# Performance work log

Hardware: AMD Instinct MI355X
Metric: run time of the kernel (lower is better)

The kernel has to match this reference:

```python
import jax, jax.numpy as jnp
import numpy as np

NUM_SLOTS = 8
SLOT_DIM = 256
ITERS = 3
EPS = 1e-8
SCALE = SLOT_DIM ** -0.5


def _ln(x, g, b, eps=1e-5):
    m = jnp.mean(x, axis=-1, keepdims=True)
    v = jnp.mean(jnp.square(x - m), axis=-1, keepdims=True)
    return (x - m) * jax.lax.rsqrt(v + eps) * g + b


def setup_inputs() -> dict:
    key = jax.random.key(0)
    ks = jax.random.split(key, 16)
    b, n, c = 32, 1024, 256
    d = SLOT_DIM
    def xavier(k, shape):
        fan_in, fan_out = shape[1], shape[0]
        lim = np.sqrt(6.0 / (fan_in + fan_out))
        return jax.random.uniform(k, shape, jnp.float32, -lim, lim)
    lim_mu = np.sqrt(6.0 / (1 + d))
    return {
        "inputs": jax.random.normal(ks[0], (b, n, c), jnp.float32),
        "noise": jax.random.normal(ks[1], (b, NUM_SLOTS, d), jnp.float32),
        "slots_mu": jax.random.uniform(ks[2], (1, 1, d), jnp.float32, -lim_mu, lim_mu),
        "slots_log_sigma": jax.random.uniform(ks[3], (1, 1, d), jnp.float32, -lim_mu, lim_mu),
        "Wq": xavier(ks[4], (d, d)),
        "Wk": xavier(ks[5], (d, c)),
        "Wv": xavier(ks[6], (d, c)),
        "gru_wih": xavier(ks[7], (3 * d, d)),
        "gru_whh": xavier(ks[8], (3 * d, d)),
        "gru_bih": jnp.zeros((3 * d,), jnp.float32),
        "gru_bhh": jnp.zeros((3 * d,), jnp.float32),
        "mlp_w1": xavier(ks[9], (4 * d, d)),
        "mlp_b1": jnp.zeros((4 * d,), jnp.float32),
        "mlp_w2": xavier(ks[10], (d, 4 * d)),
        "mlp_b2": jnp.zeros((d,), jnp.float32),
        "ln_in_g": jnp.ones((c,), jnp.float32),
        "ln_in_b": jnp.zeros((c,), jnp.float32),
        "ln_s_g": jnp.ones((d,), jnp.float32),
        "ln_s_b": jnp.zeros((d,), jnp.float32),
        "ln_ff_g": jnp.ones((d,), jnp.float32),
        "ln_ff_b": jnp.zeros((d,), jnp.float32),
    }


def reference(inputs, noise, slots_mu, slots_log_sigma, Wq, Wk, Wv,
              gru_wih, gru_whh, gru_bih, gru_bhh,
              mlp_w1, mlp_b1, mlp_w2, mlp_b2,
              ln_in_g, ln_in_b, ln_s_g, ln_s_b, ln_ff_g, ln_ff_b):
    b = inputs.shape[0]
    d = SLOT_DIM
    # slots ~ N(mu, sigma) reparameterized with given noise
    slots = slots_mu + jnp.exp(slots_log_sigma) * noise  # [b, S, d]
    x = _ln(inputs, ln_in_g, ln_in_b)
    k = jnp.einsum('bnc,dc->bnd', x, Wk)
    v = jnp.einsum('bnc,dc->bnd', x, Wv)
    for _ in range(ITERS):
        slots_prev = slots
        s = _ln(slots, ln_s_g, ln_s_b)
        q = jnp.einsum('bid,ed->bie', s, Wq)
        dots = jnp.einsum('bid,bjd->bij', q, k) * SCALE  # [b, S, n]
        attn = jax.nn.softmax(dots, axis=1) + EPS         # softmax over slots
        attn = attn / jnp.sum(attn, axis=-1, keepdims=True)
        updates = jnp.einsum('bjd,bij->bid', v, attn)      # [b, S, d]
        # GRUCell: x=updates, h=slots_prev (flattened over batch*slots)
        u = updates.reshape(-1, d)
        h = slots_prev.reshape(-1, d)
        gi = u @ gru_wih.T + gru_bih
        gh = h @ gru_whh.T + gru_bhh
        i_r, i_z, i_n = jnp.split(gi, 3, axis=-1)
        h_r, h_z, h_n = jnp.split(gh, 3, axis=-1)
        r = jax.nn.sigmoid(i_r + h_r)
        z = jax.nn.sigmoid(i_z + h_z)
        nn_ = jnp.tanh(i_n + r * h_n)
        slots = ((1.0 - z) * nn_ + z * h).reshape(b, -1, d)
        ff = _ln(slots, ln_ff_g, ln_ff_b)
        ff = jax.nn.relu(ff @ mlp_w1.T + mlp_b1) @ mlp_w2.T + mlp_b2
        slots = slots + ff
    return slots
```

## Files before the change

### kernel.cpp

```cpp
#include <hip/hip_runtime.h>


typedef __attribute__((ext_vector_type(8))) __bf16 bf16x8;
typedef __attribute__((ext_vector_type(4))) float  f32x4;

#define MFMA16(a, b, c) __builtin_amdgcn_mfma_f32_16x16x32_bf16((a), (b), (c), 0, 0, 0)

static __device__ __forceinline__ unsigned short f2bf(float f) {
    unsigned int x = __float_as_uint(f);
    x = (x + 0x7fffu + ((x >> 16) & 1u)) >> 16;
    return (unsigned short)x;
}
static __device__ __forceinline__ float bf2f(unsigned short u) {
    return __uint_as_float((unsigned int)u << 16);
}
static __device__ __forceinline__ float bflo(unsigned int x) {
    return __uint_as_float(x << 16);
}
static __device__ __forceinline__ float bfhi(unsigned int x) {
    return __uint_as_float(x & 0xffff0000u);
}

struct Params {
    const float *inputs, *noise, *mu, *ls;
    const float *Wq, *Wk, *Wv, *wih, *whh, *bih, *bhh, *w1, *b1, *w2, *b2;
    const float *ln_in_g, *ln_in_b, *ln_s_g, *ln_s_b, *ln_ff_g, *ln_ff_b;
    float* out;
    unsigned short *x_bf, *kvW_bf, *Wq_bf, *wih_bf, *whh_bf, *w1_bf, *w2_bf;
    unsigned short *kv_bf, *u_bf, *h_bf, *ff_bf, *h1_bf;
    float *slots, *q, *upart, *rspart, *gi, *gh, *opart;
};

static __device__ void qgemm(const Params& p, const unsigned short (&u)[16][264], int r0) {
    const int t = threadIdx.x, w = t >> 6, lane = t & 63;
    const int lr = lane & 15, lq = lane >> 4;
    f32x4 acc[4] = {};
    for (int k0 = 0; k0 < 256; k0 += 32) {
        bf16x8 a = *(const bf16x8*)&u[lr][k0 + lq * 8];
        #pragma unroll
        for (int j = 0; j < 4; ++j) {
            bf16x8 bv = *(const bf16x8*)(p.Wq_bf + (size_t)(w * 64 + j * 16 + lr) * 256 + k0 + lq * 8);
            acc[j] = MFMA16(a, bv, acc[j]);
        }
    }
    #pragma unroll
    for (int j = 0; j < 4; ++j)
        #pragma unroll
        for (int r = 0; r < 4; ++r)
            p.q[(size_t)(r0 + lq * 4 + r) * 256 + w * 64 + j * 16 + lr] = acc[j][r];
}

__global__ __launch_bounds__(256) void k_prep(Params p) {
    const int bid = blockIdx.x, t = threadIdx.x;
    for (int gid = bid * 256 + t; gid < 1179648; gid += 4608 * 256) {
        if      (gid <   65536) p.kvW_bf[gid]          = f2bf(p.Wk[gid]);
        else if (gid <  131072) p.kvW_bf[gid]          = f2bf(p.Wv[gid -   65536]);
        else if (gid <  196608) p.Wq_bf[gid - 131072]  = f2bf(p.Wq[gid -  131072]);
        else if (gid <  393216) p.wih_bf[gid - 196608] = f2bf(p.wih[gid - 196608]);
        else if (gid <  589824) p.whh_bf[gid - 393216] = f2bf(p.whh[gid - 393216]);
        else if (gid <  851968) p.w1_bf[gid - 589824]  = f2bf(p.w1[gid -  589824]);
        else if (gid < 1114112) p.w2_bf[gid - 851968]  = f2bf(p.w2[gid -  851968]);
        else {
            const int i = gid - 1114112;
            const int d = i & 255;
            p.slots[i] = p.mu[d] + expf(p.ls[d]) * p.noise[i];
        }
    }
    const int wid  = (bid * 256 + t) >> 6;
    const int lane = t & 63;
    const float g0 = p.ln_in_g[lane * 4 + 0], g1 = p.ln_in_g[lane * 4 + 1];
    const float g2 = p.ln_in_g[lane * 4 + 2], g3 = p.ln_in_g[lane * 4 + 3];
    const float b0 = p.ln_in_b[lane * 4 + 0], b1 = p.ln_in_b[lane * 4 + 1];
    const float b2 = p.ln_in_b[lane * 4 + 2], b3 = p.ln_in_b[lane * 4 + 3];
    #pragma unroll 2
    for (int row = wid; row < 32768; row += 18432) {
        float4 v = *(const float4*)(p.inputs + (size_t)row * 256 + lane * 4);
        float s  = v.x + v.y + v.z + v.w;
        float ss = v.x * v.x + v.y * v.y + v.z * v.z + v.w * v.w;
        #pragma unroll
        for (int o = 1; o < 64; o <<= 1) { s += __shfl_xor(s, o); ss += __shfl_xor(ss, o); }
        float mean = s * (1.f / 256.f);
        float var  = ss * (1.f / 256.f) - mean * mean;
        float rstd = rsqrtf(var + 1e-5f);
        ushort4 o4;
        o4.x = f2bf((v.x - mean) * rstd * g0 + b0);
        o4.y = f2bf((v.y - mean) * rstd * g1 + b1);
        o4.z = f2bf((v.z - mean) * rstd * g2 + b2);
        o4.w = f2bf((v.w - mean) * rstd * g3 + b3);
        *(ushort4*)(p.x_bf + (size_t)row * 256 + lane * 4) = o4;
    }
}

union KvSmem {
    struct { unsigned short As[128 * 32], Bs[128 * 32]; } g;
    unsigned short u[16][264];
};

__global__ __launch_bounds__(256) void k_kv(Params p) {
    __shared__ KvSmem sm;
    const int bid = blockIdx.x, t = threadIdx.x;
    if (bid < 1024) {
        const int m0 = (bid >> 2) * 128, n0 = (bid & 3) * 128;
        const int wave = t >> 6, lane = t & 63;
        const int qr = (wave >> 1) * 64, qc = (wave & 1) * 64;
        const int lr = lane & 15, lq = lane >> 4;
        f32x4 acc[4][4] = {};
        const int sr = t >> 2, sl = t & 3, gk = sl * 8;
        const int wsl0 = (sl ^ ((sr >> 1) & 3)) * 8;
        const int wsl1 = (sl ^ (((sr + 64) >> 1) & 3)) * 8;
        for (int k0 = 0; k0 < 256; k0 += 32) {
            __syncthreads();
            uint4 a0 = *(const uint4*)(p.x_bf   + (size_t)(m0 + sr)      * 256 + k0 + gk);
            uint4 a1 = *(const uint4*)(p.x_bf   + (size_t)(m0 + sr + 64) * 256 + k0 + gk);
            uint4 b0 = *(const uint4*)(p.kvW_bf + (size_t)(n0 + sr)      * 256 + k0 + gk);
            uint4 b1 = *(const uint4*)(p.kvW_bf + (size_t)(n0 + sr + 64) * 256 + k0 + gk);
            *(uint4*)(sm.g.As + sr * 32 + wsl0) = a0;
            *(uint4*)(sm.g.As + (sr + 64) * 32 + wsl1) = a1;
            *(uint4*)(sm.g.Bs + sr * 32 + wsl0) = b0;
            *(uint4*)(sm.g.Bs + (sr + 64) * 32 + wsl1) = b1;
            __syncthreads();
            bf16x8 af[4], bv[4];
            #pragma unroll
            for (int i = 0; i < 4; i++) {
                const int ra = qr + i * 16 + lr;
                af[i] = *(const bf16x8*)(sm.g.As + ra * 32 + ((lq ^ ((ra >> 1) & 3)) * 8));
            }
            #pragma unroll
            for (int i = 0; i < 4; i++) {
                const int rb = qc + i * 16 + lr;
                bv[i] = *(const bf16x8*)(sm.g.Bs + rb * 32 + ((lq ^ ((rb >> 1) & 3)) * 8));
            }
            #pragma unroll
            for (int i = 0; i < 4; i++)
                #pragma unroll
                for (int j = 0; j < 4; j++)
                    acc[i][j] = MFMA16(af[i], bv[j], acc[i][j]);
        }
        #pragma unroll
        for (int i = 0; i < 4; i++)
            #pragma unroll
            for (int j = 0; j < 4; j++) {
                const int col = n0 + qc + j * 16 + lr;
                #pragma unroll
                for (int r = 0; r < 4; r++) {
                    const int rw = m0 + qr + i * 16 + lq * 4 + r;
                    p.kv_bf[(size_t)rw * 512 + col] = f2bf(acc[i][j][r]);
                }
            }
    } else {
        const int r0 = (bid - 1024) * 16;
        const int row16 = t >> 4, sub = t & 15;
        float vals[16]; float s = 0.f, ss = 0.f;
        #pragma unroll
        for (int k = 0; k < 16; k += 4) {
            float4 v = *(const float4*)(p.slots + (size_t)(r0 + row16) * 256 + sub * 16 + k);
            vals[k] = v.x; vals[k + 1] = v.y; vals[k + 2] = v.z; vals[k + 3] = v.w;
            s += v.x + v.y + v.z + v.w;
            ss += v.x * v.x + v.y * v.y + v.z * v.z + v.w * v.w;
        }
        #pragma unroll
        for (int m = 1; m < 16; m <<= 1) { s += __shfl_xor(s, m); ss += __shfl_xor(ss, m); }
        const float mean = s * (1.f / 256.f);
        const float var  = ss * (1.f / 256.f) - mean * mean;
        const float rstd = rsqrtf(var + 1e-5f);
        #pragma unroll
        for (int k = 0; k < 16; ++k) {
            const int c = sub * 16 + k;
            sm.u[row16][c] = f2bf((vals[k] - mean) * rstd * p.ln_s_g[c] + p.ln_s_b[c]);
        }
        __syncthreads();
        qgemm(p, sm.u, r0);
    }
}

__global__ __launch_bounds__(256) void k_attn(Params p) {
    __shared__ float q_s[8][260];
    __shared__ float sc[8][68];
    const int bid = blockIdx.x, t = threadIdx.x;
    const int b = bid >> 4, chunk = bid & 15, j0 = chunk * 64;
    {
        const int i = t >> 5, c0 = (t & 31) * 8;
        const float* qr = p.q + (size_t)(b * 8 + i) * 256 + c0;
        *(float4*)&q_s[i][c0]     = *(const float4*)(qr);
        *(float4*)&q_s[i][c0 + 4] = *(const float4*)(qr + 4);
    }
    __syncthreads();
    {
        const int i = t & 7, jj = t >> 3;
        const float4* qrow = (const float4*)&q_s[i][0];
        #pragma unroll 1
        for (int g = 0; g < 2; ++g) {
            const int jl = g * 32 + jj;
            const uint4* krow = (const uint4*)(p.kv_bf + ((size_t)b * 1024 + j0 + jl) * 512);
            float a0 = 0, a1 = 0, a2 = 0, a3 = 0;
            #pragma unroll 8
            for (int dd = 0; dd < 32; ++dd) {
                uint4 kk = krow[dd];
                float4 q0 = qrow[2 * dd], q1 = qrow[2 * dd + 1];
                a0 += q0.x * bflo(kk.x); a1 += q0.y * bfhi(kk.x);
                a2 += q0.z * bflo(kk.y); a3 += q0.w * bfhi(kk.y);
                a0 += q1.x * bflo(kk.z); a1 += q1.y * bfhi(kk.z);
                a2 += q1.z * bflo(kk.w); a3 += q1.w * bfhi(kk.w);
            }
            sc[i][jl] = (a0 + a1 + a2 + a3) * 0.0625f;
        }
    }
    __syncthreads();
    if (t < 64) {
        float v[8], m = -1e30f;
        #pragma unroll
        for (int ii = 0; ii < 8; ++ii) { v[ii] = sc[ii][t]; m = fmaxf(m, v[ii]); }
        float s = 0.f;
        #pragma unroll
        for (int ii = 0; ii < 8; ++ii) { v[ii] = __expf(v[ii] - m); s += v[ii]; }
        const float inv = 1.f / s;
        #pragma unroll
        for (int ii = 0; ii < 8; ++ii) sc[ii][t] = v[ii] * inv + 1e-8f;
    }
    __syncthreads();
    if (t < 8) {
        float s = 0.f;
        for (int jl = 0; jl < 64; ++jl) s += sc[t][jl];
        p.rspart[((size_t)b * 16 + chunk) * 8 + t] = s;
    }
    {
        float acc[8] = {};
        const unsigned short* vbase = p.kv_bf + ((size_t)b * 1024 + j0) * 512 + 256 + t;
        #pragma unroll 8
        for (int jl = 0; jl < 64; ++jl) {
            const float vv = bf2f(vbase[(size_t)jl * 512]);
            #pragma unroll
            for (int ii = 0; ii < 8; ++ii) acc[ii] += sc[ii][jl] * vv;
        }
        float* up = p.upart + (((size_t)b * 16 + chunk) * 8) * 256 + t;
        #pragma unroll
        for (int ii = 0; ii < 8; ++ii) up[ii * 256] = acc[ii];
    }
}

__global__ __launch_bounds__(256) void k_u2b(Params p) {
    const int row = blockIdx.x, t = threadIdx.x;
    const int b = row >> 3, i = row & 7;
    float acc = 0.f, rs = 0.f;
    #pragma unroll
    for (int c = 0; c < 16; ++c) {
        acc += p.upart[(((size_t)b * 16 + c) * 8 + i) * 256 + t];
        rs  += p.rspart[((size_t)b * 16 + c) * 8 + i];
    }
    const float inv = 1.f / rs;
    p.u_bf[(size_t)row * 256 + t] = f2bf(acc * inv);
    p.h_bf[(size_t)row * 256 + t] = f2bf(p.slots[(size_t)row * 256 + t]);
}

__global__ __launch_bounds__(256) void k_gates(Params p) {
    __shared__ unsigned short As[64 * 32], Bs[64 * 32];
    const int m0 = blockIdx.x * 64;
    const int n0g = blockIdx.y * 64;
    const bool isGi = n0g < 768;
    const int n0 = isGi ? n0g : n0g - 768;
    const unsigned short* A = isGi ? p.u_bf : p.h_bf;
    const unsigned short* B = isGi ? p.wih_bf : p.whh_bf;
    float* C = isGi ? p.gi : p.gh;
    const int t = threadIdx.x, wave = t >> 6, lane = t & 63;
    const int lr = lane & 15, lq = lane >> 4;
    f32x4 acc[4] = {};
    const int sr = t >> 2, sl = t & 3, gk = sl * 8;
    const int wsl = (sl ^ ((sr >> 1) & 3)) * 8;
    for (int k0 = 0; k0 < 256; k0 += 32) {
        __syncthreads();
        uint4 a0 = *(const uint4*)(A + (size_t)(m0 + sr) * 256 + k0 + gk);
        uint4 b0 = *(const uint4*)(B + (size_t)(n0 + sr) * 256 + k0 + gk);
        *(uint4*)(As + sr * 32 + wsl) = a0;
        *(uint4*)(Bs + sr * 32 + wsl) = b0;
        __syncthreads();
        const int ra = wave * 16 + lr;
        bf16x8 af = *(const bf16x8*)(As + ra * 32 + ((lq ^ ((ra >> 1) & 3)) * 8));
        #pragma unroll
        for (int j = 0; j < 4; ++j) {
            const int rb = j * 16 + lr;
            bf16x8 bv = *(const bf16x8*)(Bs + rb * 32 + ((lq ^ ((rb >> 1) & 3)) * 8));
            acc[j] = MFMA16(af, bv, acc[j]);
        }
    }
    #pragma unroll
    for (int j = 0; j < 4; ++j) {
        const int col = n0 + j * 16 + lr;
        #pragma unroll
        for (int r = 0; r < 4; ++r) {
            const int row = m0 + wave * 16 + lq * 4 + r;
            C[(size_t)row * 768 + col] = acc[j][r];
        }
    }
}

__global__ __launch_bounds__(256) void k_gruln(Params p) {
    __shared__ float red[8];
    const int row = blockIdx.x, t = threadIdx.x;
    const float* gir = p.gi + (size_t)row * 768;
    const float* ghr = p.gh + (size_t)row * 768;
    const float ir  = gir[t]       + p.bih[t];
    const float iz  = gir[256 + t] + p.bih[256 + t];
    const float in_ = gir[512 + t] + p.bih[512 + t];
    const float hr  = ghr[t]       + p.bhh[t];
    const float hz  = ghr[256 + t] + p.bhh[256 + t];
    const float hn  = ghr[512 + t] + p.bhh[512 + t];
    const float r = 1.f / (1.f + __expf(-(ir + hr)));
    const float z = 1.f / (1.f + __expf(-(iz + hz)));
    const float n = tanhf(in_ + r * hn);
    const float h = p.slots[(size_t)row * 256 + t];
    const float s = (1.f - z) * n + z * h;
    p.slots[(size_t)row * 256 + t] = s;
    float sm = s, ssq = s * s;
    #pragma unroll
    for (int o = 32; o > 0; o >>= 1) { sm += __shfl_down(sm, o); ssq += __shfl_down(ssq, o); }
    if ((t & 63) == 0) { red[t >> 6] = sm; red[4 + (t >> 6)] = ssq; }
    __syncthreads();
    const float S  = red[0] + red[1] + red[2] + red[3];
    const float SS = red[4] + red[5] + red[6] + red[7];
    const float mean = S * (1.f / 256.f);
    const float var  = SS * (1.f / 256.f) - mean * mean;
    const float rstd = rsqrtf(var + 1e-5f);
    p.ff_bf[(size_t)row * 256 + t] = f2bf((s - mean) * rstd * p.ln_ff_g[t] + p.ln_ff_b[t]);
}

__global__ __launch_bounds__(256) void k_mlp1(Params p) {
    __shared__ unsigned short As[64 * 32], Bs[64 * 32];
    const int m0 = blockIdx.x * 64, n0 = blockIdx.y * 64;
    const int t = threadIdx.x, wave = t >> 6, lane = t & 63;
    const int lr = lane & 15, lq = lane >> 4;
    f32x4 acc[4] = {};
    const int sr = t >> 2, sl = t & 3, gk = sl * 8;
    const int wsl = (sl ^ ((sr >> 1) & 3)) * 8;
    for (int k0 = 0; k0 < 256; k0 += 32) {
        __syncthreads();
        uint4 a0 = *(const uint4*)(p.ff_bf + (size_t)(m0 + sr) * 256 + k0 + gk);
        uint4 b0 = *(const uint4*)(p.w1_bf + (size_t)(n0 + sr) * 256 + k0 + gk);
        *(uint4*)(As + sr * 32 + wsl) = a0;
        *(uint4*)(Bs + sr * 32 + wsl) = b0;
        __syncthreads();
        const int ra = wave * 16 + lr;
        bf16x8 af = *(const bf16x8*)(As + ra * 32 + ((lq ^ ((ra >> 1) & 3)) * 8));
        #pragma unroll
        for (int j = 0; j < 4; ++j) {
            const int rb = j * 16 + lr;
            bf16x8 bv = *(const bf16x8*)(Bs + rb * 32 + ((lq ^ ((rb >> 1) & 3)) * 8));
            acc[j] = MFMA16(af, bv, acc[j]);
        }
    }
    #pragma unroll
    for (int j = 0; j < 4; ++j) {
        const int col = n0 + j * 16 + lr;
        const float bb = p.b1[col];
        #pragma unroll
        for (int r = 0; r < 4; ++r) {
            const int row = m0 + wave * 16 + lq * 4 + r;
            p.h1_bf[(size_t)row * 1024 + col] = f2bf(fmaxf(acc[j][r] + bb, 0.f));
        }
    }
}

__global__ __launch_bounds__(256) void k_out(Params p) {
    __shared__ unsigned short a_s[16][264];
    const int t = threadIdx.x;
    const int r0 = blockIdx.x * 16, kb = blockIdx.y * 256;
    const int row16 = t >> 4, sub = t & 15;
    {
        const unsigned short* src = p.h1_bf + (size_t)(r0 + row16) * 1024 + kb + sub * 16;
        *(uint4*)&a_s[row16][sub * 16]     = *(const uint4*)(src);
        *(uint4*)&a_s[row16][sub * 16 + 8] = *(const uint4*)(src + 8);
    }
    __syncthreads();
    const int w = t >> 6, lane = t & 63;
    const int lr = lane & 15, lq = lane >> 4;
    f32x4 acc[4] = {};
    for (int k0 = 0; k0 < 256; k0 += 32) {
        bf16x8 a = *(const bf16x8*)&a_s[lr][k0 + lq * 8];
        #pragma unroll
        for (int j = 0; j < 4; ++j) {
            bf16x8 bv = *(const bf16x8*)(p.w2_bf + (size_t)(w * 64 + j * 16 + lr) * 1024 + kb + k0 + lq * 8);
            acc[j] = MFMA16(a, bv, acc[j]);
        }
    }
    #pragma unroll
    for (int j = 0; j < 4; ++j)
        #pragma unroll
        for (int r = 0; r < 4; ++r)
            p.opart[((size_t)blockIdx.y * 256 + r0 + lq * 4 + r) * 256 + w * 64 + j * 16 + lr] = acc[j][r];
}

template<int LAST>
__global__ __launch_bounds__(256) void k_lnq(Params p) {
    __shared__ unsigned short u[16][264];
    const int t = threadIdx.x;
    const int r0 = blockIdx.x * 16;
    const int row16 = t >> 4, sub = t & 15;
    float vals[16]; float s_ = 0.f, ss = 0.f;
    #pragma unroll
    for (int k = 0; k < 16; ++k) {
        const int c = sub * 16 + k;
        const size_t ridx = (size_t)(r0 + row16) * 256 + c;
        float v = p.opart[(size_t)(r0 + row16) * 256 + c]
                + p.opart[((size_t)256 + r0 + row16) * 256 + c]
                + p.opart[((size_t)512 + r0 + row16) * 256 + c]
                + p.opart[((size_t)768 + r0 + row16) * 256 + c]
                + p.b2[c] + p.slots[ridx];
        p.slots[ridx] = v;
        if (LAST) p.out[ridx] = v;
        vals[k] = v; s_ += v; ss += v * v;
    }
    if (LAST) return;
    #pragma unroll
    for (int m = 1; m < 16; m <<= 1) { s_ += __shfl_xor(s_, m); ss += __shfl_xor(ss, m); }
    const float mean = s_ * (1.f / 256.f);
    const float var  = ss * (1.f / 256.f) - mean * mean;
    const float rstd = rsqrtf(var + 1e-5f);
    #pragma unroll
    for (int k = 0; k < 16; ++k) {
        const int c = sub * 16 + k;
        u[row16][c] = f2bf((vals[k] - mean) * rstd * p.ln_s_g[c] + p.ln_s_b[c]);
    }
    __syncthreads();
    qgemm(p, u, r0);
}

extern "C" void kernel_launch(void* const* d_in, const int* in_sizes, int n_in,
                              void* d_out, int out_size, void* d_ws, size_t ws_size,
                              hipStream_t stream)
{
    (void)in_sizes; (void)n_in; (void)out_size; (void)ws_size;

    Params prm;
    prm.inputs  = (const float*)d_in[0];
    prm.noise   = (const float*)d_in[1];
    prm.mu      = (const float*)d_in[2];
    prm.ls      = (const float*)d_in[3];
    prm.Wq      = (const float*)d_in[4];
    prm.Wk      = (const float*)d_in[5];
    prm.Wv      = (const float*)d_in[6];
    prm.wih     = (const float*)d_in[7];
    prm.whh     = (const float*)d_in[8];
    prm.bih     = (const float*)d_in[9];
    prm.bhh     = (const float*)d_in[10];
    prm.w1      = (const float*)d_in[11];
    prm.b1      = (const float*)d_in[12];
    prm.w2      = (const float*)d_in[13];
    prm.b2      = (const float*)d_in[14];
    prm.ln_in_g = (const float*)d_in[15];
    prm.ln_in_b = (const float*)d_in[16];
    prm.ln_s_g  = (const float*)d_in[17];
    prm.ln_s_b  = (const float*)d_in[18];
    prm.ln_ff_g = (const float*)d_in[19];
    prm.ln_ff_b = (const float*)d_in[20];
    prm.out     = (float*)d_out;

    char* ptr = (char*)d_ws;
    auto alloc = [&](size_t bytes) -> char* {
        char* r = ptr; ptr += (bytes + 255) & ~(size_t)255; return r;
    };
    prm.x_bf   = (unsigned short*)alloc((size_t)32768 * 256 * 2);
    prm.kv_bf  = (unsigned short*)alloc((size_t)32768 * 512 * 2);
    prm.kvW_bf = (unsigned short*)alloc(512 * 256 * 2);
    prm.Wq_bf  = (unsigned short*)alloc(256 * 256 * 2);
    prm.wih_bf = (unsigned short*)alloc(768 * 256 * 2);
    prm.whh_bf = (unsigned short*)alloc(768 * 256 * 2);
    prm.w1_bf  = (unsigned short*)alloc(1024 * 256 * 2);
    prm.w2_bf  = (unsigned short*)alloc(256 * 1024 * 2);
    prm.slots  = (float*)         alloc(256 * 256 * 4);
    prm.q      = (float*)         alloc(256 * 256 * 4);
    prm.upart  = (float*)         alloc((size_t)32 * 16 * 8 * 256 * 4);
    prm.rspart = (float*)         alloc(32 * 16 * 8 * 4);
    prm.u_bf   = (unsigned short*)alloc(256 * 256 * 2);
    prm.h_bf   = (unsigned short*)alloc(256 * 256 * 2);
    prm.gi     = (float*)         alloc(256 * 768 * 4);
    prm.gh     = (float*)         alloc(256 * 768 * 4);
    prm.ff_bf  = (unsigned short*)alloc(256 * 256 * 2);
    prm.h1_bf  = (unsigned short*)alloc(256 * 1024 * 2);
    prm.opart  = (float*)         alloc((size_t)4 * 256 * 256 * 4);

    k_prep<<<4608, 256, 0, stream>>>(prm);
    k_kv  <<<1040, 256, 0, stream>>>(prm);
    for (int it = 0; it < 3; ++it) {
        k_attn <<<512, 256, 0, stream>>>(prm);
        k_u2b  <<<256, 256, 0, stream>>>(prm);
        k_gates<<<dim3(4, 24), 256, 0, stream>>>(prm);
        k_gruln<<<256, 256, 0, stream>>>(prm);
        k_mlp1 <<<dim3(4, 16), 256, 0, stream>>>(prm);
        k_out  <<<dim3(16, 4), 256, 0, stream>>>(prm);
        if (it < 2) k_lnq<0><<<16, 256, 0, stream>>>(prm);
        else        k_lnq<1><<<16, 256, 0, stream>>>(prm);
    }
}
```

Baseline: 293.1 us.

## Fuse slot-iteration kernels using last-block atomic reductions

```diff
diff --git a/kernel.cpp b/kernel.cpp
--- a/kernel.cpp
+++ b/kernel.cpp
@@ -27,8 +27,9 @@
     const float *ln_in_g, *ln_in_b, *ln_s_g, *ln_s_b, *ln_ff_g, *ln_ff_b;
     float* out;
     unsigned short *x_bf, *kvW_bf, *Wq_bf, *wih_bf, *whh_bf, *w1_bf, *w2_bf;
-    unsigned short *kv_bf, *u_bf, *h_bf, *ff_bf, *h1_bf;
-    float *slots, *q, *upart, *rspart, *gi, *gh, *opart;
+    unsigned short *kv_bf, *u_bf, *h_bf, *h1_bf;
+    float *slots, *smid, *q, *upart, *rspart, *gi, *gh, *opart;
+    unsigned* cnt;
 };
 
 static __device__ void qgemm(const Params& p, const unsigned short (&u)[16][264], int r0) {
@@ -166,6 +167,7 @@
         #pragma unroll
         for (int k = 0; k < 16; ++k) {
             const int c = sub * 16 + k;
+            p.h_bf[(size_t)(r0 + row16) * 256 + c] = f2bf(vals[k]);
             sm.u[row16][c] = f2bf((vals[k] - mean) * rstd * p.ln_s_g[c] + p.ln_s_b[c]);
         }
         __syncthreads();
@@ -173,11 +175,12 @@
     }
 }
 
-__global__ __launch_bounds__(256) void k_attn(Params p) {
+__global__ __launch_bounds__(256) void k_attn(Params p, int it) {
     __shared__ float q_s[8][260];
-    __shared__ float sc[8][68];
+    __shared__ float sc[8][132];
+    __shared__ int lastFlag;
     const int bid = blockIdx.x, t = threadIdx.x;
-    const int b = bid >> 4, chunk = bid & 15, j0 = chunk * 64;
+    const int b = bid >> 3, chunk = bid & 7, j0 = chunk * 128;
     {
         const int i = t >> 5, c0 = (t & 31) * 8;
         const float* qr = p.q + (size_t)(b * 8 + i) * 256 + c0;
@@ -189,7 +192,7 @@
         const int i = t & 7, jj = t >> 3;
         const float4* qrow = (const float4*)&q_s[i][0];
         #pragma unroll 1
-        for (int g = 0; g < 2; ++g) {
+        for (int g = 0; g < 4; ++g) {
             const int jl = g * 32 + jj;
             const uint4* krow = (const uint4*)(p.kv_bf + ((size_t)b * 1024 + j0 + jl) * 512);
             float a0 = 0, a1 = 0, a2 = 0, a3 = 0;
@@ -206,7 +209,7 @@
         }
     }
     __syncthreads();
-    if (t < 64) {
+    if (t < 128) {
         float v[8], m = -1e30f;
         #pragma unroll
         for (int ii = 0; ii < 8; ++ii) { v[ii] = sc[ii][t]; m = fmaxf(m, v[ii]); }
@@ -220,36 +223,43 @@
     __syncthreads();
     if (t < 8) {
         float s = 0.f;
-        for (int jl = 0; jl < 64; ++jl) s += sc[t][jl];
-        p.rspart[((size_t)b * 16 + chunk) * 8 + t] = s;
+        for (int jl = 0; jl < 128; ++jl) s += sc[t][jl];
+        p.rspart[((size_t)b * 8 + chunk) * 8 + t] = s;
     }
     {
         float acc[8] = {};
         const unsigned short* vbase = p.kv_bf + ((size_t)b * 1024 + j0) * 512 + 256 + t;
         #pragma unroll 8
-        for (int jl = 0; jl < 64; ++jl) {
+        for (int jl = 0; jl < 128; ++jl) {
             const float vv = bf2f(vbase[(size_t)jl * 512]);
             #pragma unroll
             for (int ii = 0; ii < 8; ++ii) acc[ii] += sc[ii][jl] * vv;
         }
-        float* up = p.upart + (((size_t)b * 16 + chunk) * 8) * 256 + t;
+        float* up = p.upart + (((size_t)b * 8 + chunk) * 8) * 256 + t;
         #pragma unroll
         for (int ii = 0; ii < 8; ++ii) up[ii * 256] = acc[ii];
     }
-}
-
-__global__ __launch_bounds__(256) void k_u2b(Params p) {
-    const int row = blockIdx.x, t = threadIdx.x;
-    const int b = row >> 3, i = row & 7;
-    float acc = 0.f, rs = 0.f;
-    #pragma unroll
-    for (int c = 0; c < 16; ++c) {
-        acc += p.upart[(((size_t)b * 16 + c) * 8 + i) * 256 + t];
-        rs  += p.rspart[((size_t)b * 16 + c) * 8 + i];
-    }
-    const float inv = 1.f / rs;
-    p.u_bf[(size_t)row * 256 + t] = f2bf(acc * inv);
-    p.h_bf[(size_t)row * 256 + t] = f2bf(p.slots[(size_t)row * 256 + t]);
+    __syncthreads();
+    if (t == 0) {
+        unsigned my = __hip_atomic_fetch_add(p.cnt + b * 16, 1u,
+                                             __ATOMIC_ACQ_REL, __HIP_MEMORY_SCOPE_AGENT);
+        const int isl = (my == (unsigned)(8 * (it + 1) - 1));
+        if (isl) __builtin_amdgcn_fence(__ATOMIC_ACQUIRE, "agent");
+        lastFlag = isl;
+    }
+    __syncthreads();
+    if (!lastFlag) return;
+    #pragma unroll
+    for (int i = 0; i < 8; ++i) {
+        float acc = 0.f, rs = 0.f;
+        #pragma unroll
+        for (int c = 0; c < 8; ++c) {
+            acc += p.upart[(((size_t)b * 8 + c) * 8 + i) * 256 + t];
+            rs  += p.rspart[((size_t)b * 8 + c) * 8 + i];
+        }
+        const float inv = 1.f / rs;
+        p.u_bf[(size_t)(b * 8 + i) * 256 + t] = f2bf(acc * inv);
+    }
 }
 
 __global__ __launch_bounds__(256) void k_gates(Params p) {
@@ -293,74 +303,68 @@
     }
 }
 
-__global__ __launch_bounds__(256) void k_gruln(Params p) {
-    __shared__ float red[8];
-    const int row = blockIdx.x, t = threadIdx.x;
-    const float* gir = p.gi + (size_t)row * 768;
-    const float* ghr = p.gh + (size_t)row * 768;
-    const float ir  = gir[t]       + p.bih[t];
-    const float iz  = gir[256 + t] + p.bih[256 + t];
-    const float in_ = gir[512 + t] + p.bih[512 + t];
-    const float hr  = ghr[t]       + p.bhh[t];
-    const float hz  = ghr[256 + t] + p.bhh[256 + t];
-    const float hn  = ghr[512 + t] + p.bhh[512 + t];
-    const float r = 1.f / (1.f + __expf(-(ir + hr)));
-    const float z = 1.f / (1.f + __expf(-(iz + hz)));
-    const float n = tanhf(in_ + r * hn);
-    const float h = p.slots[(size_t)row * 256 + t];
-    const float s = (1.f - z) * n + z * h;
-    p.slots[(size_t)row * 256 + t] = s;
-    float sm = s, ssq = s * s;
-    #pragma unroll
-    for (int o = 32; o > 0; o >>= 1) { sm += __shfl_down(sm, o); ssq += __shfl_down(ssq, o); }
-    if ((t & 63) == 0) { red[t >> 6] = sm; red[4 + (t >> 6)] = ssq; }
-    __syncthreads();
-    const float S  = red[0] + red[1] + red[2] + red[3];
-    const float SS = red[4] + red[5] + red[6] + red[7];
-    const float mean = S * (1.f / 256.f);
-    const float var  = SS * (1.f / 256.f) - mean * mean;
+__global__ __launch_bounds__(256) void k_mlp1f(Params p) {
+    __shared__ unsigned short ff[16][264];
+    const int t = threadIdx.x;
+    const int r0 = blockIdx.x * 16, nb = blockIdx.y * 256;
+    const int row16 = t >> 4, sub = t & 15;
+    const int grow = r0 + row16;
+    const float* gir = p.gi + (size_t)grow * 768;
+    const float* ghr = p.gh + (size_t)grow * 768;
+    float vals[16]; float s_ = 0.f, ss = 0.f;
+    #pragma unroll
+    for (int k = 0; k < 16; ++k) {
+        const int c = sub * 16 + k;
+        const float ir  = gir[c]       + p.bih[c];
+        const float iz  = gir[256 + c] + p.bih[256 + c];
+        const float in_ = gir[512 + c] + p.bih[512 + c];
+        const float hr  = ghr[c]       + p.bhh[c];
+        const float hz  = ghr[256 + c] + p.bhh[256 + c];
+        const float hn  = ghr[512 + c] + p.bhh[512 + c];
+        const float r = 1.f / (1.f + __expf(-(ir + hr)));
+        const float z = 1.f / (1.f + __expf(-(iz + hz)));
+        const float n = tanhf(in_ + r * hn);
+        const float h = p.slots[(size_t)grow * 256 + c];
+        const float s = (1.f - z) * n + z * h;
+        if (blockIdx.y == 0) p.smid[(size_t)grow * 256 + c] = s;
+        vals[k] = s; s_ += s; ss += s * s;
+    }
+    #pragma unroll
+    for (int m = 1; m < 16; m <<= 1) { s_ += __shfl_xor(s_, m); ss += __shfl_xor(ss, m); }
+    const float mean = s_ * (1.f / 256.f);
+    const float var  = ss * (1.f / 256.f) - mean * mean;
     const float rstd = rsqrtf(var + 1e-5f);
-    p.ff_bf[(size_t)row * 256 + t] = f2bf((s - mean) * rstd * p.ln_ff_g[t] + p.ln_ff_b[t]);
-}
-
-__global__ __launch_bounds__(256) void k_mlp1(Params p) {
-    __shared__ unsigned short As[64 * 32], Bs[64 * 32];
-    const int m0 = blockIdx.x * 64, n0 = blockIdx.y * 64;
-    const int t = threadIdx.x, wave = t >> 6, lane = t & 63;
-    const int lr = lane & 15, lq = lane >> 4;
+    #pragma unroll
+    for (int k = 0; k < 16; ++k) {
+        const int c = sub * 16 + k;
+        ff[row16][c] = f2bf((vals[k] - mean) * rstd * p.ln_ff_g[c] + p.ln_ff_b[c]);
+    }
+    __syncthreads();
+    const int w = t >> 6, lane = t & 63, lr = lane & 15, lq = lane >> 4;
     f32x4 acc[4] = {};
-    const int sr = t >> 2, sl = t & 3, gk = sl * 8;
-    const int wsl = (sl ^ ((sr >> 1) & 3)) * 8;
     for (int k0 = 0; k0 < 256; k0 += 32) {
-        __syncthreads();
-        uint4 a0 = *(const uint4*)(p.ff_bf + (size_t)(m0 + sr) * 256 + k0 + gk);
-        uint4 b0 = *(const uint4*)(p.w1_bf + (size_t)(n0 + sr) * 256 + k0 + gk);
-        *(uint4*)(As + sr * 32 + wsl) = a0;
-        *(uint4*)(Bs + sr * 32 + wsl) = b0;
-        __syncthreads();
-        const int ra = wave * 16 + lr;
-        bf16x8 af = *(const bf16x8*)(As + ra * 32 + ((lq ^ ((ra >> 1) & 3)) * 8));
+        bf16x8 a = *(const bf16x8*)&ff[lr][k0 + lq * 8];
         #pragma unroll
         for (int j = 0; j < 4; ++j) {
-            const int rb = j * 16 + lr;
-            bf16x8 bv = *(const bf16x8*)(Bs + rb * 32 + ((lq ^ ((rb >> 1) & 3)) * 8));
-            acc[j] = MFMA16(af, bv, acc[j]);
+            bf16x8 bv = *(const bf16x8*)(p.w1_bf + (size_t)(nb + w * 64 + j * 16 + lr) * 256 + k0 + lq * 8);
+            acc[j] = MFMA16(a, bv, acc[j]);
         }
     }
     #pragma unroll
     for (int j = 0; j < 4; ++j) {
-        const int col = n0 + j * 16 + lr;
+        const int col = nb + w * 64 + j * 16 + lr;
         const float bb = p.b1[col];
         #pragma unroll
-        for (int r = 0; r < 4; ++r) {
-            const int row = m0 + wave * 16 + lq * 4 + r;
-            p.h1_bf[(size_t)row * 1024 + col] = f2bf(fmaxf(acc[j][r] + bb, 0.f));
-        }
-    }
-}
-
-__global__ __launch_bounds__(256) void k_out(Params p) {
+        for (int r = 0; r < 4; ++r)
+            p.h1_bf[(size_t)(r0 + lq * 4 + r) * 1024 + col] = f2bf(fmaxf(acc[j][r] + bb, 0.f));
+    }
+}
+
+template<int LAST>
+__global__ __launch_bounds__(256) void k_out(Params p, int it) {
     __shared__ unsigned short a_s[16][264];
+    __shared__ unsigned short u[16][264];
+    __shared__ int lastFlag;
     const int t = threadIdx.x;
     const int r0 = blockIdx.x * 16, kb = blockIdx.y * 256;
     const int row16 = t >> 4, sub = t & 15;
@@ -370,8 +374,7 @@
         *(uint4*)&a_s[row16][sub * 16 + 8] = *(const uint4*)(src + 8);
     }
     __syncthreads();
-    const int w = t >> 6, lane = t & 63;
-    const int lr = lane & 15, lq = lane >> 4;
+    const int w = t >> 6, lane = t & 63, lr = lane & 15, lq = lane >> 4;
     f32x4 acc[4] = {};
     for (int k0 = 0; k0 < 256; k0 += 32) {
         bf16x8 a = *(const bf16x8*)&a_s[lr][k0 + lq * 8];
@@ -386,26 +389,31 @@
         #pragma unroll
         for (int r = 0; r < 4; ++r)
             p.opart[((size_t)blockIdx.y * 256 + r0 + lq * 4 + r) * 256 + w * 64 + j * 16 + lr] = acc[j][r];
-}
-
-template<int LAST>
-__global__ __launch_bounds__(256) void k_lnq(Params p) {
-    __shared__ unsigned short u[16][264];
-    const int t = threadIdx.x;
-    const int r0 = blockIdx.x * 16;
-    const int row16 = t >> 4, sub = t & 15;
+    __syncthreads();
+    if (t == 0) {
+        unsigned my = __hip_atomic_fetch_add(p.cnt + (32 + blockIdx.x) * 16, 1u,
+                                             __ATOMIC_ACQ_REL, __HIP_MEMORY_SCOPE_AGENT);
+        const int isl = (my == (unsigned)(4 * (it + 1) - 1));
+        if (isl) __builtin_amdgcn_fence(__ATOMIC_ACQUIRE, "agent");
+        lastFlag = isl;
+    }
+    __syncthreads();
+    if (!lastFlag) return;
     float vals[16]; float s_ = 0.f, ss = 0.f;
     #pragma unroll
     for (int k = 0; k < 16; ++k) {
         const int c = sub * 16 + k;
         const size_t ridx = (size_t)(r0 + row16) * 256 + c;
-        float v = p.opart[(size_t)(r0 + row16) * 256 + c]
+        float v = p.opart[ridx]
                 + p.opart[((size_t)256 + r0 + row16) * 256 + c]
                 + p.opart[((size_t)512 + r0 + row16) * 256 + c]
                 + p.opart[((size_t)768 + r0 + row16) * 256 + c]
-                + p.b2[c] + p.slots[ridx];
-        p.slots[ridx] = v;
-        if (LAST) p.out[ridx] = v;
+                + p.b2[c] + p.smid[ridx];
+        if (LAST) { p.out[ridx] = v; }
+        else {
+            p.slots[ridx] = v;
+            p.h_bf[ridx]  = f2bf(v);
+        }
         vals[k] = v; s_ += v; ss += v * v;
     }
     if (LAST) return;
@@ -457,6 +465,7 @@
     auto alloc = [&](size_t bytes) -> char* {
         char* r = ptr; ptr += (bytes + 255) & ~(size_t)255; return r;
     };
+    prm.cnt    = (unsigned*)      alloc(4096);
     prm.x_bf   = (unsigned short*)alloc((size_t)32768 * 256 * 2);
     prm.kv_bf  = (unsigned short*)alloc((size_t)32768 * 512 * 2);
     prm.kvW_bf = (unsigned short*)alloc(512 * 256 * 2);
@@ -466,27 +475,25 @@
     prm.w1_bf  = (unsigned short*)alloc(1024 * 256 * 2);
     prm.w2_bf  = (unsigned short*)alloc(256 * 1024 * 2);
     prm.slots  = (float*)         alloc(256 * 256 * 4);
+    prm.smid   = (float*)         alloc(256 * 256 * 4);
     prm.q      = (float*)         alloc(256 * 256 * 4);
-    prm.upart  = (float*)         alloc((size_t)32 * 16 * 8 * 256 * 4);
-    prm.rspart = (float*)         alloc(32 * 16 * 8 * 4);
+    prm.upart  = (float*)         alloc((size_t)32 * 8 * 8 * 256 * 4);
+    prm.rspart = (float*)         alloc(32 * 8 * 8 * 4);
     prm.u_bf   = (unsigned short*)alloc(256 * 256 * 2);
     prm.h_bf   = (unsigned short*)alloc(256 * 256 * 2);
     prm.gi     = (float*)         alloc(256 * 768 * 4);
     prm.gh     = (float*)         alloc(256 * 768 * 4);
-    prm.ff_bf  = (unsigned short*)alloc(256 * 256 * 2);
     prm.h1_bf  = (unsigned short*)alloc(256 * 1024 * 2);
     prm.opart  = (float*)         alloc((size_t)4 * 256 * 256 * 4);
 
+    hipMemsetAsync(prm.cnt, 0, 4096, stream);
     k_prep<<<4608, 256, 0, stream>>>(prm);
     k_kv  <<<1040, 256, 0, stream>>>(prm);
     for (int it = 0; it < 3; ++it) {
-        k_attn <<<512, 256, 0, stream>>>(prm);
-        k_u2b  <<<256, 256, 0, stream>>>(prm);
+        k_attn <<<256, 256, 0, stream>>>(prm, it);
         k_gates<<<dim3(4, 24), 256, 0, stream>>>(prm);
-        k_gruln<<<256, 256, 0, stream>>>(prm);
-        k_mlp1 <<<dim3(4, 16), 256, 0, stream>>>(prm);
-        k_out  <<<dim3(16, 4), 256, 0, stream>>>(prm);
-        if (it < 2) k_lnq<0><<<16, 256, 0, stream>>>(prm);
-        else        k_lnq<1><<<16, 256, 0, stream>>>(prm);
-    }
-}
+        k_mlp1f<<<dim3(16, 4), 256, 0, stream>>>(prm);
+        if (it < 2) k_out<0><<<dim3(16, 4), 256, 0, stream>>>(prm, it);
+        else        k_out<1><<<dim3(16, 4), 256, 0, stream>>>(prm, it);
+    }
+}
```

Result: slower. 406.9 us (+38.8%).

## Fuse hidden-gate GEMM into attention kernel and fold partial reduction into input-gate GEMM

Applied to the files above, without the earlier changes.

```diff
diff --git a/kernel.cpp b/kernel.cpp
--- a/kernel.cpp
+++ b/kernel.cpp
@@ -27,7 +27,7 @@
     const float *ln_in_g, *ln_in_b, *ln_s_g, *ln_s_b, *ln_ff_g, *ln_ff_b;
     float* out;
     unsigned short *x_bf, *kvW_bf, *Wq_bf, *wih_bf, *whh_bf, *w1_bf, *w2_bf;
-    unsigned short *kv_bf, *u_bf, *h_bf, *ff_bf, *h1_bf;
+    unsigned short *kv_bf, *h_bf, *ff_bf, *h1_bf;
     float *slots, *q, *upart, *rspart, *gi, *gh, *opart;
 };
 
@@ -166,6 +166,7 @@
         #pragma unroll
         for (int k = 0; k < 16; ++k) {
             const int c = sub * 16 + k;
+            p.h_bf[(size_t)(r0 + row16) * 256 + c] = f2bf(vals[k]);
             sm.u[row16][c] = f2bf((vals[k] - mean) * rstd * p.ln_s_g[c] + p.ln_s_b[c]);
         }
         __syncthreads();
@@ -173,108 +174,145 @@
     }
 }
 
-__global__ __launch_bounds__(256) void k_attn(Params p) {
-    __shared__ float q_s[8][260];
-    __shared__ float sc[8][68];
+union AtSmem {
+    struct { float q[8][260]; float sc[8][132]; } at;
+    struct { unsigned short As[64 * 32], Bs[64 * 32]; } g;
+};
+
+__global__ __launch_bounds__(256) void k_attn_gh(Params p) {
+    __shared__ AtSmem sm;
     const int bid = blockIdx.x, t = threadIdx.x;
-    const int b = bid >> 4, chunk = bid & 15, j0 = chunk * 64;
-    {
-        const int i = t >> 5, c0 = (t & 31) * 8;
-        const float* qr = p.q + (size_t)(b * 8 + i) * 256 + c0;
-        *(float4*)&q_s[i][c0]     = *(const float4*)(qr);
-        *(float4*)&q_s[i][c0 + 4] = *(const float4*)(qr + 4);
+    if (bid < 256) {
+        const int b = bid >> 3, chunk = bid & 7, j0 = chunk * 128;
+        {
+            const int i = t >> 5, c0 = (t & 31) * 8;
+            const float* qr = p.q + (size_t)(b * 8 + i) * 256 + c0;
+            *(float4*)&sm.at.q[i][c0]     = *(const float4*)(qr);
+            *(float4*)&sm.at.q[i][c0 + 4] = *(const float4*)(qr + 4);
+        }
+        __syncthreads();
+        {
+            const int i = t & 7, jj = t >> 3;
+            const float4* qrow = (const float4*)&sm.at.q[i][0];
+            #pragma unroll 1
+            for (int g = 0; g < 4; ++g) {
+                const int jl = g * 32 + jj;
+                const uint4* krow = (const uint4*)(p.kv_bf + ((size_t)b * 1024 + j0 + jl) * 512);
+                float a0 = 0, a1 = 0, a2 = 0, a3 = 0;
+                #pragma unroll 8
+                for (int dd = 0; dd < 32; ++dd) {
+                    uint4 kk = krow[dd];
+                    float4 q0 = qrow[2 * dd], q1 = qrow[2 * dd + 1];
+                    a0 += q0.x * bflo(kk.x); a1 += q0.y * bfhi(kk.x);
+                    a2 += q0.z * bflo(kk.y); a3 += q0.w * bfhi(kk.y);
+                    a0 += q1.x * bflo(kk.z); a1 += q1.y * bfhi(kk.z);
+                    a2 += q1.z * bflo(kk.w); a3 += q1.w * bfhi(kk.w);
+                }
+                sm.at.sc[i][jl] = (a0 + a1 + a2 + a3) * 0.0625f;
+            }
+        }
+        __syncthreads();
+        if (t < 128) {
+            float v[8], m = -1e30f;
+            #pragma unroll
+            for (int ii = 0; ii < 8; ++ii) { v[ii] = sm.at.sc[ii][t]; m = fmaxf(m, v[ii]); }
+            float s = 0.f;
+            #pragma unroll
+            for (int ii = 0; ii < 8; ++ii) { v[ii] = __expf(v[ii] - m); s += v[ii]; }
+            const float inv = 1.f / s;
+            #pragma unroll
+            for (int ii = 0; ii < 8; ++ii) sm.at.sc[ii][t] = v[ii] * inv + 1e-8f;
+        }
+        __syncthreads();
+        if (t < 8) {
+            float s = 0.f;
+            for (int jl = 0; jl < 128; ++jl) s += sm.at.sc[t][jl];
+            p.rspart[((size_t)b * 8 + chunk) * 8 + t] = s;
+        }
+        {
+            float acc[8] = {};
+            const unsigned short* vbase = p.kv_bf + ((size_t)b * 1024 + j0) * 512 + 256 + t;
+            #pragma unroll 8
+            for (int jl = 0; jl < 128; ++jl) {
+                const float vv = bf2f(vbase[(size_t)jl * 512]);
+                #pragma unroll
+                for (int ii = 0; ii < 8; ++ii) acc[ii] += sm.at.sc[ii][jl] * vv;
+            }
+            float* up = p.upart + (((size_t)b * 8 + chunk) * 8) * 256 + t;
+            #pragma unroll
+            for (int ii = 0; ii < 8; ++ii) up[ii * 256] = acc[ii];
+        }
+    } else {
+        const int g = bid - 256;
+        const int m0 = (g & 3) * 64, n0 = (g >> 2) * 64;
+        const int wave = t >> 6, lane = t & 63;
+        const int lr = lane & 15, lq = lane >> 4;
+        f32x4 acc[4] = {};
+        const int sr = t >> 2, sl = t & 3, gk = sl * 8;
+        const int wsl = (sl ^ ((sr >> 1) & 3)) * 8;
+        for (int k0 = 0; k0 < 256; k0 += 32) {
+            __syncthreads();
+            uint4 a0 = *(const uint4*)(p.h_bf   + (size_t)(m0 + sr) * 256 + k0 + gk);
+            uint4 b0 = *(const uint4*)(p.whh_bf + (size_t)(n0 + sr) * 256 + k0 + gk);
+            *(uint4*)(sm.g.As + sr * 32 + wsl) = a0;
+            *(uint4*)(sm.g.Bs + sr * 32 + wsl) = b0;
+            __syncthreads();
+            const int ra = wave * 16 + lr;
+            bf16x8 af = *(const bf16x8*)(sm.g.As + ra * 32 + ((lq ^ ((ra >> 1) & 3)) * 8));
+            #pragma unroll
+            for (int j = 0; j < 4; ++j) {
+                const int rb = j * 16 + lr;
+                bf16x8 bv = *(const bf16x8*)(sm.g.Bs + rb * 32 + ((lq ^ ((rb >> 1) & 3)) * 8));
+                acc[j] = MFMA16(af, bv, acc[j]);
+            }
+        }
+        #pragma unroll
+        for (int j = 0; j < 4; ++j) {
+            const int col = n0 + j * 16 + lr;
+            #pragma unroll
+            for (int r = 0; r < 4; ++r)
+                p.gh[(size_t)(m0 + wave * 16 + lq * 4 + r) * 768 + col] = acc[j][r];
+        }
+    }
+}
+
+__global__ __launch_bounds__(256) void k_gi(Params p) {
+    __shared__ unsigned short uS[8][2048];
+    __shared__ unsigned short Bs[64 * 32];
+    __shared__ float rs_l[64];
+    const int t = threadIdx.x;
+    const int m0 = blockIdx.x * 64, n0 = blockIdx.y * 64;
+    if (t < 64) {
+        const int grow = m0 + t, b = grow >> 3, i = grow & 7;
+        float rs = 0.f;
+        #pragma unroll
+        for (int c = 0; c < 8; ++c) rs += p.rspart[((size_t)b * 8 + c) * 8 + i];
+        rs_l[t] = 1.f / rs;
     }
     __syncthreads();
     {
-        const int i = t & 7, jj = t >> 3;
-        const float4* qrow = (const float4*)&q_s[i][0];
-        #pragma unroll 1
-        for (int g = 0; g < 2; ++g) {
-            const int jl = g * 32 + jj;
-            const uint4* krow = (const uint4*)(p.kv_bf + ((size_t)b * 1024 + j0 + jl) * 512);
-            float a0 = 0, a1 = 0, a2 = 0, a3 = 0;
-            #pragma unroll 8
-            for (int dd = 0; dd < 32; ++dd) {
-                uint4 kk = krow[dd];
-                float4 q0 = qrow[2 * dd], q1 = qrow[2 * dd + 1];
-                a0 += q0.x * bflo(kk.x); a1 += q0.y * bfhi(kk.x);
-                a2 += q0.z * bflo(kk.y); a3 += q0.w * bfhi(kk.y);
-                a0 += q1.x * bflo(kk.z); a1 += q1.y * bfhi(kk.z);
-                a2 += q1.z * bflo(kk.w); a3 += q1.w * bfhi(kk.w);
-            }
-            sc[i][jl] = (a0 + a1 + a2 + a3) * 0.0625f;
-        }
-    }
-    __syncthreads();
-    if (t < 64) {
-        float v[8], m = -1e30f;
-        #pragma unroll
-        for (int ii = 0; ii < 8; ++ii) { v[ii] = sc[ii][t]; m = fmaxf(m, v[ii]); }
-        float s = 0.f;
-        #pragma unroll
-        for (int ii = 0; ii < 8; ++ii) { v[ii] = __expf(v[ii] - m); s += v[ii]; }
-        const float inv = 1.f / s;
-        #pragma unroll
-        for (int ii = 0; ii < 8; ++ii) sc[ii][t] = v[ii] * inv + 1e-8f;
-    }
-    __syncthreads();
-    if (t < 8) {
-        float s = 0.f;
-        for (int jl = 0; jl < 64; ++jl) s += sc[t][jl];
-        p.rspart[((size_t)b * 16 + chunk) * 8 + t] = s;
-    }
-    {
-        float acc[8] = {};
-        const unsigned short* vbase = p.kv_bf + ((size_t)b * 1024 + j0) * 512 + 256 + t;
-        #pragma unroll 8
-        for (int jl = 0; jl < 64; ++jl) {
-            const float vv = bf2f(vbase[(size_t)jl * 512]);
-            #pragma unroll
-            for (int ii = 0; ii < 8; ++ii) acc[ii] += sc[ii][jl] * vv;
-        }
-        float* up = p.upart + (((size_t)b * 16 + chunk) * 8) * 256 + t;
-        #pragma unroll
-        for (int ii = 0; ii < 8; ++ii) up[ii * 256] = acc[ii];
-    }
-}
-
-__global__ __launch_bounds__(256) void k_u2b(Params p) {
-    const int row = blockIdx.x, t = threadIdx.x;
-    const int b = row >> 3, i = row & 7;
-    float acc = 0.f, rs = 0.f;
-    #pragma unroll
-    for (int c = 0; c < 16; ++c) {
-        acc += p.upart[(((size_t)b * 16 + c) * 8 + i) * 256 + t];
-        rs  += p.rspart[((size_t)b * 16 + c) * 8 + i];
-    }
-    const float inv = 1.f / rs;
-    p.u_bf[(size_t)row * 256 + t] = f2bf(acc * inv);
-    p.h_bf[(size_t)row * 256 + t] = f2bf(p.slots[(size_t)row * 256 + t]);
-}
-
-__global__ __launch_bounds__(256) void k_gates(Params p) {
-    __shared__ unsigned short As[64 * 32], Bs[64 * 32];
-    const int m0 = blockIdx.x * 64;
-    const int n0g = blockIdx.y * 64;
-    const bool isGi = n0g < 768;
-    const int n0 = isGi ? n0g : n0g - 768;
-    const unsigned short* A = isGi ? p.u_bf : p.h_bf;
-    const unsigned short* B = isGi ? p.wih_bf : p.whh_bf;
-    float* C = isGi ? p.gi : p.gh;
-    const int t = threadIdx.x, wave = t >> 6, lane = t & 63;
+        const int sl = (t >> 3) & 3, kc = t >> 5, k7 = t & 7;
+        for (int r = 0; r < 64; ++r) {
+            const int grow = m0 + r, b = grow >> 3, i = grow & 7;
+            float a = 0.f;
+            #pragma unroll
+            for (int c = 0; c < 8; ++c)
+                a += p.upart[(((size_t)b * 8 + c) * 8 + i) * 256 + t];
+            uS[kc][r * 32 + ((sl ^ ((r >> 1) & 3)) * 8) + k7] = f2bf(a * rs_l[r]);
+        }
+    }
+    const int wave = t >> 6, lane = t & 63;
     const int lr = lane & 15, lq = lane >> 4;
     f32x4 acc[4] = {};
-    const int sr = t >> 2, sl = t & 3, gk = sl * 8;
-    const int wsl = (sl ^ ((sr >> 1) & 3)) * 8;
+    const int sr = t >> 2, sl2 = t & 3, gk = sl2 * 8;
+    const int wsl = (sl2 ^ ((sr >> 1) & 3)) * 8;
     for (int k0 = 0; k0 < 256; k0 += 32) {
         __syncthreads();
-        uint4 a0 = *(const uint4*)(A + (size_t)(m0 + sr) * 256 + k0 + gk);
-        uint4 b0 = *(const uint4*)(B + (size_t)(n0 + sr) * 256 + k0 + gk);
-        *(uint4*)(As + sr * 32 + wsl) = a0;
+        uint4 b0 = *(const uint4*)(p.wih_bf + (size_t)(n0 + sr) * 256 + k0 + gk);
         *(uint4*)(Bs + sr * 32 + wsl) = b0;
         __syncthreads();
         const int ra = wave * 16 + lr;
-        bf16x8 af = *(const bf16x8*)(As + ra * 32 + ((lq ^ ((ra >> 1) & 3)) * 8));
+        bf16x8 af = *(const bf16x8*)(uS[k0 >> 5] + ra * 32 + ((lq ^ ((ra >> 1) & 3)) * 8));
         #pragma unroll
         for (int j = 0; j < 4; ++j) {
             const int rb = j * 16 + lr;
@@ -286,10 +324,8 @@
     for (int j = 0; j < 4; ++j) {
         const int col = n0 + j * 16 + lr;
         #pragma unroll
-        for (int r = 0; r < 4; ++r) {
-            const int row = m0 + wave * 16 + lq * 4 + r;
-            C[(size_t)row * 768 + col] = acc[j][r];
-        }
+        for (int r = 0; r < 4; ++r)
+            p.gi[(size_t)(m0 + wave * 16 + lq * 4 + r) * 768 + col] = acc[j][r];
     }
 }
 
@@ -404,8 +440,11 @@
                 + p.opart[((size_t)512 + r0 + row16) * 256 + c]
                 + p.opart[((size_t)768 + r0 + row16) * 256 + c]
                 + p.b2[c] + p.slots[ridx];
-        p.slots[ridx] = v;
-        if (LAST) p.out[ridx] = v;
+        if (LAST) { p.out[ridx] = v; }
+        else {
+            p.slots[ridx] = v;
+            p.h_bf[ridx]  = f2bf(v);
+        }
         vals[k] = v; s_ += v; ss += v * v;
     }
     if (LAST) return;
@@ -467,9 +506,8 @@
     prm.w2_bf  = (unsigned short*)alloc(256 * 1024 * 2);
     prm.slots  = (float*)         alloc(256 * 256 * 4);
     prm.q      = (float*)         alloc(256 * 256 * 4);
-    prm.upart  = (float*)         alloc((size_t)32 * 16 * 8 * 256 * 4);
-    prm.rspart = (float*)         alloc(32 * 16 * 8 * 4);
-    prm.u_bf   = (unsigned short*)alloc(256 * 256 * 2);
+    prm.upart  = (float*)         alloc((size_t)32 * 8 * 8 * 256 * 4);
+    prm.rspart = (float*)         alloc(32 * 8 * 8 * 4);
     prm.h_bf   = (unsigned short*)alloc(256 * 256 * 2);
     prm.gi     = (float*)         alloc(256 * 768 * 4);
     prm.gh     = (float*)         alloc(256 * 768 * 4);
@@ -480,12 +518,11 @@
     k_prep<<<4608, 256, 0, stream>>>(prm);
     k_kv  <<<1040, 256, 0, stream>>>(prm);
     for (int it = 0; it < 3; ++it) {
-        k_attn <<<512, 256, 0, stream>>>(prm);
-        k_u2b  <<<256, 256, 0, stream>>>(prm);
-        k_gates<<<dim3(4, 24), 256, 0, stream>>>(prm);
-        k_gruln<<<256, 256, 0, stream>>>(prm);
-        k_mlp1 <<<dim3(4, 16), 256, 0, stream>>>(prm);
-        k_out  <<<dim3(16, 4), 256, 0, stream>>>(prm);
+        k_attn_gh<<<304, 256, 0, stream>>>(prm);
+        k_gi     <<<dim3(4, 12), 256, 0, stream>>>(prm);
+        k_gruln  <<<256, 256, 0, stream>>>(prm);
+        k_mlp1   <<<dim3(4, 16), 256, 0, stream>>>(prm);
+        k_out    <<<dim3(16, 4), 256, 0, stream>>>(prm);
         if (it < 2) k_lnq<0><<<16, 256, 0, stream>>>(prm);
         else        k_lnq<1><<<16, 256, 0, stream>>>(prm);
     }
```

Result: slower. 356.9 us (+21.8%).
